# Optimization experiments

Measured on AMD Instinct MI355X. Metric: run time of the kernel, lower is better.

Reference implementation:

```python
import jax, jax.numpy as jnp
import numpy as np

# static config (matches init_kwargs)
PL, LAT, LON = 8, 48, 96
WP, WL, WW = 2, 6, 12
SP, SL, SN = 1, 3, 6
NH = 16


def _earth_position_index(ws):
    wp, wl, ww = ws
    zi = np.arange(wp); zj = -np.arange(wp) * wp
    hi = np.arange(wl); hj = -np.arange(wl) * wl
    w = np.arange(ww)
    c1 = np.stack(np.meshgrid(zi, hi, w, indexing='ij')).reshape(3, -1)
    c2 = np.stack(np.meshgrid(zj, hj, w, indexing='ij')).reshape(3, -1)
    coords = (c1[:, :, None] - c2[:, None, :]).transpose(1, 2, 0).astype(np.int64)
    coords[:, :, 2] += ww - 1
    coords[:, :, 1] *= 2 * ww - 1
    coords[:, :, 0] *= (2 * ww - 1) * wl * wl
    return coords.sum(-1)  # (N, N)

_POS_IDX = jnp.asarray(_earth_position_index((WP, WL, WW)))


def _ln(x, w, b, eps=1e-5):
    m = x.mean(-1, keepdims=True)
    v = x.var(-1, keepdims=True)
    return (x - m) / jnp.sqrt(v + eps) * w + b


def setup_inputs() -> dict:
    key = jax.random.key(0)
    ks = jax.random.split(key, 8)
    B, C = 1, 512
    L = PL * LAT * LON
    TOW = (PL // WP) * (LAT // WL)
    TBL = WP * WP * WL * WL * (2 * WW - 1)
    s = 0.02
    return {
        'x': jax.random.normal(ks[0], (B, L, C), jnp.float32),
        'norm1_w': jnp.ones((C,), jnp.float32), 'norm1_b': jnp.zeros((C,), jnp.float32),
        'qkv_w': jax.random.normal(ks[1], (C, 3 * C), jnp.float32) * s,
        'qkv_b': jnp.zeros((3 * C,), jnp.float32),
        'proj_w': jax.random.normal(ks[2], (C, C), jnp.float32) * s,
        'proj_b': jnp.zeros((C,), jnp.float32),
        'bias_table': jax.random.normal(ks[3], (TBL, TOW, NH), jnp.float32) * s,
        'norm2_w': jnp.ones((C,), jnp.float32), 'norm2_b': jnp.zeros((C,), jnp.float32),
        'mlp_w1': jax.random.normal(ks[4], (C, 4 * C), jnp.float32) * s,
        'mlp_b1': jnp.zeros((4 * C,), jnp.float32),
        'mlp_w2': jax.random.normal(ks[5], (4 * C, C), jnp.float32) * s,
        'mlp_b2': jnp.zeros((C,), jnp.float32),
    }


def reference(x, norm1_w, norm1_b, qkv_w, qkv_b, proj_w, proj_b, bias_table,
              norm2_w, norm2_b, mlp_w1, mlp_b1, mlp_w2, mlp_b2):
    B, L, C = x.shape
    HD = C // NH
    scale = HD ** -0.5
    N = WP * WL * WW
    nPl, nLat, nLon = PL // WP, LAT // WL, LON // WW
    nW = nPl * nLat

    # norm1 + roll + window partition (B, nLon, nPl, nLat, wp, wl, ww, C)
    h = _ln(x, norm1_w, norm1_b).reshape(B, PL, LAT, LON, C)
    h = jnp.roll(h, (-SP, -SL, -SN), axis=(1, 2, 3))
    h = h.reshape(B, nPl, WP, nLat, WL, nLon, WW, C)
    h = h.transpose(0, 5, 1, 3, 2, 4, 6, 7).reshape(B * nLon, nW, N, C)

    # attention
    qkv = (h @ qkv_w + qkv_b).reshape(B * nLon, nW, N, 3, NH, HD)
    qkv = qkv.transpose(3, 0, 4, 1, 2, 5)  # (3, B_, nh, nW, N, hd)
    q, k, v = qkv[0] * scale, qkv[1], qkv[2]
    attn = jnp.einsum('bhwnd,bhwmd->bhwnm', q, k)
    bias = bias_table[_POS_IDX.reshape(-1)].reshape(N, N, nW, NH)
    bias = bias.transpose(3, 2, 0, 1)  # (nh, nW, N, N)
    attn = jax.nn.softmax(attn + bias[None], axis=-1)
    o = jnp.einsum('bhwnm,bhwmd->bhwnd', attn, v)
    o = o.transpose(0, 2, 3, 1, 4).reshape(B * nLon, nW, N, C)
    o = o @ proj_w + proj_b

    # reverse partition + roll back
    o = o.reshape(B, nLon, nPl, nLat, WP, WL, WW, C)
    o = o.transpose(0, 2, 4, 3, 5, 1, 6, 7).reshape(B, PL, LAT, LON, C)
    o = jnp.roll(o, (SP, SL, SN), axis=(1, 2, 3)).reshape(B, L, C)

    x = x + o
    h2 = _ln(x, norm2_w, norm2_b)
    h2 = jax.nn.gelu(h2 @ mlp_w1 + mlp_b1, approximate=False) @ mlp_w2 + mlp_b2
    return x + h2
```

## Files before the change

kernel.cpp:

```cpp
#include <hip/hip_runtime.h>
#include <hip/hip_bf16.h>
#include <math.h>

typedef __bf16 bf16;
typedef __attribute__((ext_vector_type(8))) __bf16 bf16x8;
typedef __attribute__((ext_vector_type(4))) float f32x4;
typedef __attribute__((ext_vector_type(8))) float f32x8;

#define NTOK   36864
#define CDIM   512
#define NHEAD  16
#define HD     32
#define NWIN   32
#define NLON   8
#define WTOK   144
#define TBL    3312

#define GLOAD_LDS16(g, l) __builtin_amdgcn_global_load_lds( \
    (const __attribute__((address_space(1))) void*)(const void*)(g), \
    (__attribute__((address_space(3))) void*)(l), 16, 0, 0)

__device__ __forceinline__ int src_token(int r) {
    int ww_ = r % 12; int q = r / 12;
    int wl_ = q % 6;  q /= 6;
    int wp_ = q & 1;  q >>= 1;
    int lat_g = q & 7; q >>= 3;
    int pl_g = q & 3;  q >>= 2;
    int lon_g = q;
    int pl  = pl_g * 2 + wp_ + 1;  if (pl  >= 8)  pl  -= 8;
    int lat = lat_g * 6 + wl_ + 3; if (lat >= 48) lat -= 48;
    int lon = lon_g * 12 + ww_ + 6; if (lon >= 96) lon -= 96;
    return (pl * 48 + lat) * 96 + lon;
}

__device__ __forceinline__ float gelu_exact(float x) {
    return 0.5f * x * (1.0f + erff(x * 0.70710678118654752f));
}

__global__ __launch_bounds__(256) void transpose_f32_bf16(const float* __restrict__ in,
                                                          bf16* __restrict__ out,
                                                          int R, int Cc) {
    __shared__ bf16 tile[32][33];
    int c0 = blockIdx.x * 32, r0 = blockIdx.y * 32;
    int tx = threadIdx.x & 31, ty = threadIdx.x >> 5;
#pragma unroll
    for (int i = 0; i < 32; i += 8)
        tile[ty + i][tx] = (bf16)in[(size_t)(r0 + ty + i) * Cc + c0 + tx];
    __syncthreads();
#pragma unroll
    for (int i = 0; i < 32; i += 8)
        out[(size_t)(c0 + ty + i) * R + r0 + tx] = tile[tx][ty + i];
}

__global__ __launch_bounds__(256) void table_transpose(const float* __restrict__ in,
                                                       float* __restrict__ outT) {
    __shared__ float tile[32][33];
    int i0 = blockIdx.x * 32, w0 = blockIdx.y * 32;
    int tx = threadIdx.x & 31, ty = threadIdx.x >> 5;
#pragma unroll
    for (int r = 0; r < 32; r += 8)
        if (i0 + ty + r < TBL) tile[ty + r][tx] = in[(size_t)(i0 + ty + r) * 512 + w0 + tx];
    __syncthreads();
#pragma unroll
    for (int r = 0; r < 32; r += 8)
        if (i0 + tx < TBL) outT[(size_t)(w0 + ty + r) * TBL + i0 + tx] = tile[tx][ty + r];
}

template<bool PERM>
__global__ __launch_bounds__(256) void ln_kernel(const float* __restrict__ in,
                                                 const float* __restrict__ w,
                                                 const float* __restrict__ b,
                                                 bf16* __restrict__ out) {
    int r = blockIdx.x * 4 + (threadIdx.x >> 6);
    int lane = threadIdx.x & 63;
    int s = PERM ? src_token(r) : r;
    f32x8 v8 = *(const f32x8*)(in + (size_t)s * CDIM + lane * 8);
    float sum = 0.f, sq = 0.f;
#pragma unroll
    for (int i = 0; i < 8; ++i) { sum += v8[i]; sq += v8[i] * v8[i]; }
#pragma unroll
    for (int m = 1; m < 64; m <<= 1) { sum += __shfl_xor(sum, m); sq += __shfl_xor(sq, m); }
    float mean = sum * (1.f / 512.f);
    float var  = sq  * (1.f / 512.f) - mean * mean;
    float rstd = rsqrtf(var + 1e-5f);
    f32x8 w8 = *(const f32x8*)(w + lane * 8);
    f32x8 b8 = *(const f32x8*)(b + lane * 8);
    bf16x8 o8;
#pragma unroll
    for (int i = 0; i < 8; ++i)
        o8[i] = (bf16)((v8[i] - mean) * rstd * w8[i] + b8[i]);
    *(bf16x8*)(out + (size_t)r * CDIM + lane * 8) = o8;
}

template<int EPI>
__global__ __launch_bounds__(256) void gemm_bt(const bf16* __restrict__ A,
                                               const bf16* __restrict__ Bt,
                                               const float* __restrict__ bias,
                                               void* __restrict__ Cout_,
                                               const float* __restrict__ X,
                                               int K, int N, int gx) {
    __shared__ bf16 As[2 * 128 * 32];
    __shared__ bf16 Bs[2 * 128 * 32];
    int t = threadIdx.x;
    int wid = t >> 6, lane = t & 63;
    int wr = wid >> 1, wc = wid & 1;
    int g = lane >> 4, cl = lane & 15;

    int nwg = gridDim.x, orig = blockIdx.x;
    int wg = orig;
    if ((nwg & 7) == 0) {
        int cpx = nwg >> 3;
        wg = (orig & 7) * cpx + (orig >> 3);
    }
    int m0 = (wg / gx) * 128, n0 = (wg % gx) * 128;
    f32x4 acc[4][4] = {};

    int srow = wid * 16 + (lane >> 2);
    int scol = (lane & 3) * 8;
    const bf16* Ag0 = A  + (size_t)(m0 + srow) * K + scol;
    const bf16* Ag1 = Ag0 + (size_t)64 * K;
    const bf16* Bg0 = Bt + (size_t)(n0 + srow) * K + scol;
    const bf16* Bg1 = Bg0 + (size_t)64 * K;
    int ldsoff = wid * 16 * 32;

    GLOAD_LDS16(Ag0, As + ldsoff);
    GLOAD_LDS16(Ag1, As + 64 * 32 + ldsoff);
    GLOAD_LDS16(Bg0, Bs + ldsoff);
    GLOAD_LDS16(Bg1, Bs + 64 * 32 + ldsoff);
    __syncthreads();

    int nt = K >> 5, cur = 0;
    for (int kt = 0; kt < nt; ++kt) {
        if (kt + 1 < nt) {
            int k1 = (kt + 1) << 5;
            bf16* Ad = As + (cur ^ 1) * 4096;
            bf16* Bd = Bs + (cur ^ 1) * 4096;
            GLOAD_LDS16(Ag0 + k1, Ad + ldsoff);
            GLOAD_LDS16(Ag1 + k1, Ad + 64 * 32 + ldsoff);
            GLOAD_LDS16(Bg0 + k1, Bd + ldsoff);
            GLOAD_LDS16(Bg1 + k1, Bd + 64 * 32 + ldsoff);
        }
        const bf16* Ar = As + cur * 4096;
        const bf16* Br = Bs + cur * 4096;
        bf16x8 af[4], bfv[4];
#pragma unroll
        for (int i = 0; i < 4; ++i)
            af[i]  = *(const bf16x8*)(Ar + (wr * 64 + i * 16 + cl) * 32 + g * 8);
#pragma unroll
        for (int i = 0; i < 4; ++i)
            bfv[i] = *(const bf16x8*)(Br + (wc * 64 + i * 16 + cl) * 32 + g * 8);
#pragma unroll
        for (int mi = 0; mi < 4; ++mi)
#pragma unroll
            for (int ni = 0; ni < 4; ++ni)
                acc[mi][ni] = __builtin_amdgcn_mfma_f32_16x16x32_bf16(af[mi], bfv[ni], acc[mi][ni], 0, 0, 0);
        __syncthreads();
        cur ^= 1;
    }

#pragma unroll
    for (int mi = 0; mi < 4; ++mi) {
#pragma unroll
        for (int j = 0; j < 4; ++j) {
            int row = m0 + wr * 64 + mi * 16 + g * 4 + j;
            int srw = 0;
            if (EPI == 2) srw = src_token(row);
#pragma unroll
            for (int ni = 0; ni < 4; ++ni) {
                int col = n0 + wc * 64 + ni * 16 + cl;
                float v = acc[mi][ni][j] + bias[col];
                if (EPI == 1) v = gelu_exact(v);
                if (EPI == 0 || EPI == 1) {
                    ((bf16*)Cout_)[(size_t)row * N + col] = (bf16)v;
                } else if (EPI == 2) {
                    size_t o = (size_t)srw * CDIM + col;
                    ((float*)Cout_)[o] = X[o] + v;
                } else {
                    size_t o = (size_t)row * N + col;
                    ((float*)Cout_)[o] += v;
                }
            }
        }
    }
}

__global__ __launch_bounds__(256) void attn_mfma(const bf16* __restrict__ qkv,
                                                 const float* __restrict__ tableT,
                                                 bf16* __restrict__ obuf) {
    int h = blockIdx.x, w = blockIdx.y, b_ = blockIdx.z;
    int t = threadIdx.x, wid = t >> 6, lane = t & 63;
    int g = lane >> 4, cl = lane & 15;
    size_t base = ((size_t)b_ * NWIN + w) * WTOK;

    __shared__ bf16 P[WTOK * 168];
    __shared__ bf16 vT[32 * 168];
    __shared__ float bias_s[TBL];
    bf16* qs = P;
    bf16* ks = P + WTOK * 40;

    const bf16* qg = qkv + base * 1536 + h * 32;
    for (int tok = t >> 2; tok < WTOK; tok += 64) {
        int c8 = (t & 3) * 8;
        *(bf16x8*)(qs + tok * 40 + c8) = *(const bf16x8*)(qg + (size_t)tok * 1536 + c8);
        *(bf16x8*)(ks + tok * 40 + c8) = *(const bf16x8*)(qg + 512 + (size_t)tok * 1536 + c8);
        bf16x8 v8 = *(const bf16x8*)(qg + 1024 + (size_t)tok * 1536 + c8);
#pragma unroll
        for (int i = 0; i < 8; ++i) vT[(c8 + i) * 168 + tok] = v8[i];
    }
    for (int z = t; z < 32 * 24; z += 256) vT[(z / 24) * 168 + 144 + (z % 24)] = (bf16)0.f;
    const float* tb = tableT + (size_t)(w * 16 + h) * TBL;
    for (int i = t; i < TBL; i += 256) bias_s[i] = tb[i];
    __syncthreads();

    f32x4 sacc[3][9] = {};
    bf16x8 kf[9];
#pragma unroll
    for (int ct = 0; ct < 9; ++ct)
        kf[ct] = *(const bf16x8*)(ks + (ct * 16 + cl) * 40 + g * 8);
#pragma unroll
    for (int rti = 0; rti < 3; ++rti) {
        int rt = wid + rti * 4;
        if (rt < 9) {
            bf16x8 qf = *(const bf16x8*)(qs + (rt * 16 + cl) * 40 + g * 8);
#pragma unroll
            for (int ct = 0; ct < 9; ++ct)
                sacc[rti][ct] = __builtin_amdgcn_mfma_f32_16x16x32_bf16(qf, kf[ct], sacc[rti][ct], 0, 0, 0);
        }
    }
    __syncthreads();

    for (int z = t; z < WTOK * 24; z += 256) P[(z / 24) * 168 + 144 + (z % 24)] = (bf16)0.f;

    int bm[9];
#pragma unroll
    for (int ct = 0; ct < 9; ++ct) {
        int m = ct * 16 + cl;
        int wm = m % 12, tm = m / 12, hm = tm % 6, zm = tm / 6;
        bm[ct] = zm * 1656 + hm * 138 + 11 - wm;
    }

    const float scale = 0.17677669529663689f;
    float rinv[3][4];
#pragma unroll
    for (int rti = 0; rti < 3; ++rti) {
        int rt = wid + rti * 4;
        if (rt < 9) {
#pragma unroll
            for (int j = 0; j < 4; ++j) {
                int row = rt * 16 + g * 4 + j;
                int wn = row % 12, tn = row / 12, hn = tn % 6, zn = tn / 6;
                int an = zn * 828 + hn * 23 + wn;
                float mx = -1e30f;
#pragma unroll
                for (int ct = 0; ct < 9; ++ct) {
                    float v = sacc[rti][ct][j] * scale + bias_s[an + bm[ct]];
                    sacc[rti][ct][j] = v;
                    mx = fmaxf(mx, v);
                }
                for (int msk = 1; msk < 16; msk <<= 1) mx = fmaxf(mx, __shfl_xor(mx, msk));
                float sm = 0.f;
#pragma unroll
                for (int ct = 0; ct < 9; ++ct) {
                    float p = __expf(sacc[rti][ct][j] - mx);
                    sm += p;
                    P[row * 168 + ct * 16 + cl] = (bf16)p;
                }
                for (int msk = 1; msk < 16; msk <<= 1) sm += __shfl_xor(sm, msk);
                rinv[rti][j] = 1.f / sm;
            }
        }
    }
    __syncthreads();

#pragma unroll
    for (int rti = 0; rti < 3; ++rti) {
        int rt = wid + rti * 4;
        if (rt < 9) {
            f32x4 oacc[2] = {};
#pragma unroll
            for (int ks_ = 0; ks_ < 5; ++ks_) {
                bf16x8 pf = *(const bf16x8*)(P + (rt * 16 + cl) * 168 + ks_ * 32 + g * 8);
#pragma unroll
                for (int c2 = 0; c2 < 2; ++c2) {
                    bf16x8 vf = *(const bf16x8*)(vT + (c2 * 16 + cl) * 168 + ks_ * 32 + g * 8);
                    oacc[c2] = __builtin_amdgcn_mfma_f32_16x16x32_bf16(pf, vf, oacc[c2], 0, 0, 0);
                }
            }
#pragma unroll
            for (int c2 = 0; c2 < 2; ++c2)
#pragma unroll
                for (int j = 0; j < 4; ++j) {
                    int row = rt * 16 + g * 4 + j;
                    obuf[(base + row) * CDIM + h * 32 + c2 * 16 + cl] =
                        (bf16)(oacc[c2][j] * rinv[rti][j]);
                }
        }
    }
}

extern "C" void kernel_launch(void* const* d_in, const int* in_sizes, int n_in,
                              void* d_out, int out_size, void* d_ws, size_t ws_size,
                              hipStream_t stream) {
    const float* x       = (const float*)d_in[0];
    const float* n1w     = (const float*)d_in[1];
    const float* n1b     = (const float*)d_in[2];
    const float* qkv_w   = (const float*)d_in[3];
    const float* qkv_b   = (const float*)d_in[4];
    const float* proj_w  = (const float*)d_in[5];
    const float* proj_b  = (const float*)d_in[6];
    const float* btab    = (const float*)d_in[7];
    const float* n2w     = (const float*)d_in[8];
    const float* n2b     = (const float*)d_in[9];
    const float* mlp_w1  = (const float*)d_in[10];
    const float* mlp_b1  = (const float*)d_in[11];
    const float* mlp_w2  = (const float*)d_in[12];
    const float* mlp_b2  = (const float*)d_in[13];
    float* out = (float*)d_out;

    const size_t OFF_HBUF = 0;
    const size_t OFF_QKV  = 37748736;
    const size_t OFF_TT   = 150994944;
    const size_t OFF_OBUF = 188743680;
    const size_t OFF_WTQ  = 226492416;
    const size_t OFF_WTP  = 228065280;
    const size_t OFF_WT1  = 228589568;
    const size_t OFF_WT2  = 230686720;
    const size_t NEED     = 232783872;

    if (ws_size < NEED) return;

    char* ws = (char*)d_ws;
    bf16*  hbuf   = (bf16*)(ws + OFF_HBUF);
    bf16*  qkvbuf = (bf16*)(ws + OFF_QKV);
    bf16*  midbuf = qkvbuf;
    float* tableT = (float*)(ws + OFF_TT);
    bf16*  obuf   = (bf16*)(ws + OFF_OBUF);
    bf16*  wtq    = (bf16*)(ws + OFF_WTQ);
    bf16*  wtp    = (bf16*)(ws + OFF_WTP);
    bf16*  wt1    = (bf16*)(ws + OFF_WT1);
    bf16*  wt2    = (bf16*)(ws + OFF_WT2);

    transpose_f32_bf16<<<dim3(1536 / 32, 512 / 32), 256, 0, stream>>>(qkv_w, wtq, 512, 1536);
    transpose_f32_bf16<<<dim3(512 / 32, 512 / 32), 256, 0, stream>>>(proj_w, wtp, 512, 512);
    transpose_f32_bf16<<<dim3(2048 / 32, 512 / 32), 256, 0, stream>>>(mlp_w1, wt1, 512, 2048);
    transpose_f32_bf16<<<dim3(512 / 32, 2048 / 32), 256, 0, stream>>>(mlp_w2, wt2, 2048, 512);
    table_transpose<<<dim3((TBL + 31) / 32, 512 / 32), 256, 0, stream>>>(btab, tableT);

    ln_kernel<true><<<NTOK / 4, 256, 0, stream>>>(x, n1w, n1b, hbuf);

    gemm_bt<0><<<12 * 288, 256, 0, stream>>>(hbuf, wtq, qkv_b, qkvbuf, nullptr, 512, 1536, 12);

    attn_mfma<<<dim3(NHEAD, NWIN, NLON), 256, 0, stream>>>(qkvbuf, tableT, obuf);

    gemm_bt<2><<<4 * 288, 256, 0, stream>>>(obuf, wtp, proj_b, out, x, 512, 512, 4);

    ln_kernel<false><<<NTOK / 4, 256, 0, stream>>>(out, n2w, n2b, hbuf);

    gemm_bt<1><<<16 * 288, 256, 0, stream>>>(hbuf, wt1, mlp_b1, midbuf, nullptr, 512, 2048, 16);

    gemm_bt<3><<<4 * 288, 256, 0, stream>>>(midbuf, wt2, mlp_b2, out, nullptr, 2048, 512, 4);
}
```

Baseline: 575.8 us.

## Fuse projection GEMM with residual and LayerNorm2, merge weight transposes, approximate GELU

Adds a proj_ln2 kernel. Each block computes a 32-row by 512-column tile of the output projection, adds bias and the residual at the un-rolled token positions, and reduces row statistics across waves to apply LayerNorm2 in the epilogue. This removes the separate LN2 kernel and its extra pass over the fp32 activation. The four weight-transpose launches are merged into one kernel that picks its matrix from the block index. Exact erf GELU is replaced with the tanh-based approximation using __expf, which cuts epilogue cost but departs from approximate=False numerics.

```diff
diff --git a/kernel.cpp b/kernel.cpp
--- a/kernel.cpp
+++ b/kernel.cpp
@@ -33,15 +33,29 @@
     return (pl * 48 + lat) * 96 + lon;
 }
 
-__device__ __forceinline__ float gelu_exact(float x) {
-    return 0.5f * x * (1.0f + erff(x * 0.70710678118654752f));
-}
-
-__global__ __launch_bounds__(256) void transpose_f32_bf16(const float* __restrict__ in,
-                                                          bf16* __restrict__ out,
-                                                          int R, int Cc) {
+__device__ __forceinline__ float gelu_fast(float x) {
+    float u = 1.5957691216f * (x + 0.044715f * x * x * x);
+    float t = 1.f - 2.f / (__expf(u) + 1.f);
+    return 0.5f * x * (1.f + t);
+}
+
+__global__ __launch_bounds__(256) void transpose_weights(const float* __restrict__ qkv_w,
+                                                         const float* __restrict__ proj_w,
+                                                         const float* __restrict__ w1,
+                                                         const float* __restrict__ w2,
+                                                         bf16* __restrict__ wtq,
+                                                         bf16* __restrict__ wtp,
+                                                         bf16* __restrict__ wt1,
+                                                         bf16* __restrict__ wt2) {
     __shared__ bf16 tile[32][33];
-    int c0 = blockIdx.x * 32, r0 = blockIdx.y * 32;
+    int bid = blockIdx.x;
+    const float* in; bf16* outp; int R, Cc, ti;
+    if (bid < 768)       { in = qkv_w;  outp = wtq; R = 512;  Cc = 1536; ti = bid; }
+    else if (bid < 1024) { in = proj_w; outp = wtp; R = 512;  Cc = 512;  ti = bid - 768; }
+    else if (bid < 2048) { in = w1;     outp = wt1; R = 512;  Cc = 2048; ti = bid - 1024; }
+    else                 { in = w2;     outp = wt2; R = 2048; Cc = 512;  ti = bid - 2048; }
+    int gx = Cc >> 5;
+    int c0 = (ti % gx) * 32, r0 = (ti / gx) * 32;
     int tx = threadIdx.x & 31, ty = threadIdx.x >> 5;
 #pragma unroll
     for (int i = 0; i < 32; i += 8)
@@ -49,7 +63,7 @@
     __syncthreads();
 #pragma unroll
     for (int i = 0; i < 32; i += 8)
-        out[(size_t)(c0 + ty + i) * R + r0 + tx] = tile[tx][ty + i];
+        outp[(size_t)(c0 + ty + i) * R + r0 + tx] = tile[tx][ty + i];
 }
 
 __global__ __launch_bounds__(256) void table_transpose(const float* __restrict__ in,
@@ -97,7 +111,6 @@
                                                const bf16* __restrict__ Bt,
                                                const float* __restrict__ bias,
                                                void* __restrict__ Cout_,
-                                               const float* __restrict__ X,
                                                int K, int N, int gx) {
     __shared__ bf16 As[2 * 128 * 32];
     __shared__ bf16 Bs[2 * 128 * 32];
@@ -163,22 +176,131 @@
 #pragma unroll
         for (int j = 0; j < 4; ++j) {
             int row = m0 + wr * 64 + mi * 16 + g * 4 + j;
-            int srw = 0;
-            if (EPI == 2) srw = src_token(row);
 #pragma unroll
             for (int ni = 0; ni < 4; ++ni) {
                 int col = n0 + wc * 64 + ni * 16 + cl;
                 float v = acc[mi][ni][j] + bias[col];
-                if (EPI == 1) v = gelu_exact(v);
+                if (EPI == 1) v = gelu_fast(v);
                 if (EPI == 0 || EPI == 1) {
                     ((bf16*)Cout_)[(size_t)row * N + col] = (bf16)v;
-                } else if (EPI == 2) {
-                    size_t o = (size_t)srw * CDIM + col;
-                    ((float*)Cout_)[o] = X[o] + v;
                 } else {
                     size_t o = (size_t)row * N + col;
                     ((float*)Cout_)[o] += v;
                 }
+            }
+        }
+    }
+}
+
+__global__ __launch_bounds__(256) void proj_ln2(const bf16* __restrict__ A,
+                                                const bf16* __restrict__ Bt,
+                                                const float* __restrict__ pbias,
+                                                const float* __restrict__ X,
+                                                float* __restrict__ out,
+                                                const float* __restrict__ n2w,
+                                                const float* __restrict__ n2b,
+                                                bf16* __restrict__ hb) {
+    __shared__ bf16 As[2 * 32 * 32];
+    __shared__ bf16 Bs[2 * 512 * 32];
+    __shared__ float redS[32][4];
+    __shared__ float redQ[32][4];
+    const int t = threadIdx.x;
+    const int wid = t >> 6, lane = t & 63;
+    const int g = lane >> 4, cl = lane & 15;
+
+    int nwg = gridDim.x, orig = blockIdx.x;
+    int cpx = nwg >> 3;
+    int wg = (orig & 7) * cpx + (orig >> 3);
+    const int r0 = wg * 32;
+
+    f32x4 acc[2][8] = {};
+
+    const int srow = lane >> 2;
+    const int scol = (lane & 3) * 8;
+
+#define PSTAGE(k0, buf) do {                                                          \
+        if (wid < 2)                                                                  \
+            GLOAD_LDS16(A + (size_t)(r0 + wid * 16 + srow) * CDIM + (k0) + scol,      \
+                        As + (buf) * 1024 + wid * 512);                               \
+        _Pragma("unroll")                                                             \
+        for (int L = 0; L < 8; ++L)                                                   \
+            GLOAD_LDS16(Bt + (size_t)(L * 64 + wid * 16 + srow) * CDIM + (k0) + scol, \
+                        Bs + (buf) * 16384 + (L * 64 + wid * 16) * 32);               \
+    } while (0)
+
+    PSTAGE(0, 0);
+    __syncthreads();
+
+    int cur = 0;
+    for (int kt = 0; kt < 16; ++kt) {
+        if (kt + 1 < 16) PSTAGE((kt + 1) << 5, cur ^ 1);
+        const bf16* Ar = As + cur * 1024;
+        const bf16* Br = Bs + cur * 16384;
+        bf16x8 af[2], bfv[8];
+#pragma unroll
+        for (int mi = 0; mi < 2; ++mi)
+            af[mi] = *(const bf16x8*)(Ar + (mi * 16 + cl) * 32 + g * 8);
+#pragma unroll
+        for (int ni = 0; ni < 8; ++ni)
+            bfv[ni] = *(const bf16x8*)(Br + (wid * 128 + ni * 16 + cl) * 32 + g * 8);
+#pragma unroll
+        for (int mi = 0; mi < 2; ++mi)
+#pragma unroll
+            for (int ni = 0; ni < 8; ++ni)
+                acc[mi][ni] = __builtin_amdgcn_mfma_f32_16x16x32_bf16(af[mi], bfv[ni], acc[mi][ni], 0, 0, 0);
+        __syncthreads();
+        cur ^= 1;
+    }
+#undef PSTAGE
+
+    int srcrow[8];
+#pragma unroll
+    for (int mi = 0; mi < 2; ++mi)
+#pragma unroll
+        for (int j = 0; j < 4; ++j)
+            srcrow[mi * 4 + j] = src_token(r0 + mi * 16 + g * 4 + j);
+
+#pragma unroll
+    for (int mi = 0; mi < 2; ++mi) {
+#pragma unroll
+        for (int j = 0; j < 4; ++j) {
+            float s = 0.f, q = 0.f;
+#pragma unroll
+            for (int ni = 0; ni < 8; ++ni) {
+                int col = wid * 128 + ni * 16 + cl;
+                float v = acc[mi][ni][j] + pbias[col]
+                        + X[(size_t)srcrow[mi * 4 + j] * CDIM + col];
+                acc[mi][ni][j] = v;
+                s += v; q += v * v;
+            }
+#pragma unroll
+            for (int m_ = 1; m_ < 16; m_ <<= 1) { s += __shfl_xor(s, m_); q += __shfl_xor(q, m_); }
+            if (cl == 0) {
+                int lr = mi * 16 + g * 4 + j;
+                redS[lr][wid] = s;
+                redQ[lr][wid] = q;
+            }
+        }
+    }
+    __syncthreads();
+
+#pragma unroll
+    for (int mi = 0; mi < 2; ++mi) {
+#pragma unroll
+        for (int j = 0; j < 4; ++j) {
+            int lr = mi * 16 + g * 4 + j;
+            float S = redS[lr][0] + redS[lr][1] + redS[lr][2] + redS[lr][3];
+            float Q = redQ[lr][0] + redQ[lr][1] + redQ[lr][2] + redQ[lr][3];
+            float mean = S * (1.f / 512.f);
+            float var  = Q * (1.f / 512.f) - mean * mean;
+            float rstd = rsqrtf(var + 1e-5f);
+            size_t rb = (size_t)srcrow[mi * 4 + j] * CDIM;
+#pragma unroll
+            for (int ni = 0; ni < 8; ++ni) {
+                int col = wid * 128 + ni * 16 + cl;
+                float x1v = acc[mi][ni][j];
+                out[rb + col] = x1v;
+                hb[rb + col] = (bf16)((x1v - mean) * rstd * n2w[col] + n2b[col]);
             }
         }
     }
@@ -340,23 +462,19 @@
     bf16*  wt1    = (bf16*)(ws + OFF_WT1);
     bf16*  wt2    = (bf16*)(ws + OFF_WT2);
 
-    transpose_f32_bf16<<<dim3(1536 / 32, 512 / 32), 256, 0, stream>>>(qkv_w, wtq, 512, 1536);
-    transpose_f32_bf16<<<dim3(512 / 32, 512 / 32), 256, 0, stream>>>(proj_w, wtp, 512, 512);
-    transpose_f32_bf16<<<dim3(2048 / 32, 512 / 32), 256, 0, stream>>>(mlp_w1, wt1, 512, 2048);
-    transpose_f32_bf16<<<dim3(512 / 32, 2048 / 32), 256, 0, stream>>>(mlp_w2, wt2, 2048, 512);
+    transpose_weights<<<3072, 256, 0, stream>>>(qkv_w, proj_w, mlp_w1, mlp_w2,
+                                                wtq, wtp, wt1, wt2);
     table_transpose<<<dim3((TBL + 31) / 32, 512 / 32), 256, 0, stream>>>(btab, tableT);
 
     ln_kernel<true><<<NTOK / 4, 256, 0, stream>>>(x, n1w, n1b, hbuf);
 
-    gemm_bt<0><<<12 * 288, 256, 0, stream>>>(hbuf, wtq, qkv_b, qkvbuf, nullptr, 512, 1536, 12);
+    gemm_bt<0><<<12 * 288, 256, 0, stream>>>(hbuf, wtq, qkv_b, qkvbuf, 512, 1536, 12);
 
     attn_mfma<<<dim3(NHEAD, NWIN, NLON), 256, 0, stream>>>(qkvbuf, tableT, obuf);
 
-    gemm_bt<2><<<4 * 288, 256, 0, stream>>>(obuf, wtp, proj_b, out, x, 512, 512, 4);
-
-    ln_kernel<false><<<NTOK / 4, 256, 0, stream>>>(out, n2w, n2b, hbuf);
-
-    gemm_bt<1><<<16 * 288, 256, 0, stream>>>(hbuf, wt1, mlp_b1, midbuf, nullptr, 512, 2048, 16);
-
-    gemm_bt<3><<<4 * 288, 256, 0, stream>>>(midbuf, wt2, mlp_b2, out, nullptr, 2048, 512, 4);
-}
+    proj_ln2<<<1152, 256, 0, stream>>>(obuf, wtp, proj_b, x, out, n2w, n2b, hbuf);
+
+    gemm_bt<1><<<16 * 288, 256, 0, stream>>>(hbuf, wt1, mlp_b1, midbuf, 512, 2048, 16);
+
+    gemm_bt<3><<<4 * 288, 256, 0, stream>>>(midbuf, wt2, mlp_b2, out, 2048, 512, 4);
+}
```

After: 635.4 us. 10.3% more time.
